# Kernel optimization log

Measured on AMD Instinct MI355X. Metric: run time of the kernel, lower is better.

The kernel has to match this reference:

```python
import jax, jax.numpy as jnp
import numpy as np
import math

B, T, DM = 2, 2048, 2048
H, D = 16, 128
HALF = D // 2


def _rope_tables(T, half, base=10000.0):
    inv_freq = 1.0 / (base ** (np.arange(0, half, dtype=np.float32) / half))
    t = np.arange(T, dtype=np.float32)
    freqs = np.outer(t, inv_freq)  # [T, half]
    return jnp.asarray(np.cos(freqs)), jnp.asarray(np.sin(freqs))


def setup_inputs() -> dict:
    key = jax.random.key(0)
    ks = jax.random.split(key, 5)
    s = 1.0 / math.sqrt(DM)
    x = jax.random.normal(ks[0], (B, T, DM), dtype=jnp.float32)
    wq = jax.random.normal(ks[1], (H * D, DM), dtype=jnp.float32) * s
    wk = jax.random.normal(ks[2], (H * D, DM), dtype=jnp.float32) * s
    wv = jax.random.normal(ks[3], (H * D, DM), dtype=jnp.float32) * s
    wo = jax.random.normal(ks[4], (DM, H * D), dtype=jnp.float32) * s
    cos, sin = _rope_tables(T, HALF)
    return {"x": x, "wq": wq, "wk": wk, "wv": wv, "wo": wo, "cos": cos, "sin": sin}


def _apply_rope(x, cos, sin):
    # x: [B,H,T,D]; cos/sin: [T, D//2] broadcast over batch and head
    x1, x2 = x[..., :HALF], x[..., HALF:]
    c = cos[None, None]
    s = sin[None, None]
    return jnp.concatenate([x1 * c - x2 * s, x1 * s + x2 * c], axis=-1)


def reference(x, wq, wk, wv, wo, cos, sin):
    Bx, Tx, _ = x.shape
    # QKV projections (Linear with weight [out,in]): y = x @ W^T
    q = jnp.einsum('btd,ed->bte', x, wq).reshape(Bx, Tx, H, D).transpose(0, 2, 1, 3)
    k = jnp.einsum('btd,ed->bte', x, wk).reshape(Bx, Tx, H, D).transpose(0, 2, 1, 3)
    v = jnp.einsum('btd,ed->bte', x, wv).reshape(Bx, Tx, H, D).transpose(0, 2, 1, 3)
    q = _apply_rope(q, cos, sin)
    k = _apply_rope(k, cos, sin)
    # causal SDPA (prefill path: kv_cache=None, mask='causal')
    scale = 1.0 / math.sqrt(D)
    scores = jnp.einsum('bhqd,bhkd->bhqk', q, k) * scale  # [B,H,T,T]
    causal = jnp.tril(jnp.ones((Tx, Tx), dtype=bool))
    scores = jnp.where(causal[None, None], scores, jnp.finfo(scores.dtype).min)
    attn = jax.nn.softmax(scores, axis=-1)
    out = jnp.einsum('bhqk,bhkd->bhqd', attn, v)  # [B,H,T,D]
    out = out.transpose(0, 2, 1, 3).reshape(Bx, Tx, H * D)
    return jnp.einsum('bte,de->btd', out, wo)
```

## Files before the change

kernel.cpp:

```cpp
#include <hip/hip_runtime.h>

typedef __attribute__((ext_vector_type(8))) short short8;
typedef __attribute__((ext_vector_type(4))) float floatx4;

#define B_ 2
#define T_ 2048
#define DM_ 2048
#define H_ 16
#define D_ 128
#define HALF_ 64

__device__ inline unsigned short f2bf(float f) {
    union { float f; unsigned u; } v; v.f = f;
    unsigned r = (v.u + 0x7fffu + ((v.u >> 16) & 1u)) >> 16;
    return (unsigned short)r;
}

__device__ inline void gld16(const void* g, void* l) {
    __builtin_amdgcn_global_load_lds(
        (__attribute__((address_space(1))) void*)g,
        (__attribute__((address_space(3))) void*)l,
        16, 0, 0);
}

__global__ void conv_all(const float* __restrict__ x,
                         const float* __restrict__ w0, const float* __restrict__ w1,
                         const float* __restrict__ w2, const float* __restrict__ w3,
                         unsigned short* __restrict__ xb,
                         unsigned short* __restrict__ wb, int n4w) {
    int y = blockIdx.y;
    int i = blockIdx.x * 256 + threadIdx.x;
    const float* src;
    ushort4* dst;
    if (y < 2) { src = x + (size_t)y * n4w * 4; dst = (ushort4*)xb + (size_t)y * n4w; }
    else {
        src = (y == 2) ? w0 : (y == 3) ? w1 : (y == 4) ? w2 : w3;
        dst = (ushort4*)wb + (size_t)(y - 2) * n4w;
    }
    float4 f = ((const float4*)src)[i];
    ushort4 o;
    o.x = f2bf(f.x); o.y = f2bf(f.y); o.z = f2bf(f.z); o.w = f2bf(f.w);
    dst[i] = o;
}

__global__ __launch_bounds__(256)
void gemm_qkv(const unsigned short* __restrict__ A,
              const unsigned short* __restrict__ W,
              unsigned short* __restrict__ q,
              unsigned short* __restrict__ k,
              unsigned short* __restrict__ vt,
              const float* __restrict__ cosT,
              const float* __restrict__ sinT) {
    __shared__ unsigned short sh[18432];
    unsigned short* As = sh;
    unsigned short* Bs = sh + 8192;

    const int t    = threadIdx.x;
    const int lane = t & 63;
    const int w    = t >> 6;
    const int wm   = w >> 1, wn = w & 1;
    const int l15  = lane & 15, quad = lane >> 4;
    const int bx   = blockIdx.x;
    const int row0 = blockIdx.y * 128;
    const int colg0 = bx * 128;
    const int h     = bx & 15;
    const int K = DM_;

    floatx4 acc[4][4];
    for (int i = 0; i < 4; ++i)
        for (int j = 0; j < 4; ++j)
            acc[i][j] = (floatx4){0.f, 0.f, 0.f, 0.f};

    for (int kt = 0; kt < K / 64; ++kt) {
        if (kt) __syncthreads();
        for (int i = 0; i < 4; ++i) {
            int g  = i * 256 + t;
            int g0 = i * 256 + (t & ~63);
            int m  = g >> 3, c = g & 7;
            int k8 = c ^ (m & 7);
            gld16(A + (size_t)(row0 + m) * K + kt * 64 + k8 * 8, As + (size_t)g0 * 8);
            gld16(W + (size_t)(colg0 + m) * K + kt * 64 + k8 * 8, Bs + (size_t)g0 * 8);
        }
        __syncthreads();

        for (int s = 0; s < 2; ++s) {
            short8 a[4], b[4];
            for (int mf = 0; mf < 4; ++mf) {
                int row = wm * 64 + mf * 16 + l15;
                int pc  = (quad + s * 4) ^ (row & 7);
                a[mf] = *(const short8*)(As + row * 64 + pc * 8);
            }
            for (int nf = 0; nf < 4; ++nf) {
                int row = wn * 32 + (nf & 1) * 16 + (nf >> 1) * 64 + l15;
                int pc  = (quad + s * 4) ^ (row & 7);
                b[nf] = *(const short8*)(Bs + row * 64 + pc * 8);
            }
            for (int mf = 0; mf < 4; ++mf)
                for (int nf = 0; nf < 4; ++nf)
                    acc[mf][nf] = __builtin_amdgcn_mfma_f32_16x16x32_bf16(
                        a[mf], b[nf], acc[mf][nf], 0, 0, 0);
        }
    }

    if (bx < 32) {
        unsigned short* C = (bx < 16) ? q : k;
        for (int mf = 0; mf < 4; ++mf) {
            for (int nf = 0; nf < 2; ++nf) {
                int dh = wn * 32 + nf * 16 + l15;
                for (int r = 0; r < 4; ++r) {
                    int rowg = row0 + wm * 64 + mf * 16 + quad * 4 + r;
                    int tt = rowg & 2047;
                    float c = cosT[tt * 64 + dh];
                    float s = sinT[tt * 64 + dh];
                    float x1 = acc[mf][nf][r];
                    float x2 = acc[mf][nf + 2][r];
                    size_t base = (size_t)rowg * DM_ + h * D_ + dh;
                    C[base]         = f2bf(x1 * c - x2 * s);
                    C[base + HALF_] = f2bf(x1 * s + x2 * c);
                }
            }
        }
    } else {
        __syncthreads();
        unsigned short* P = sh + w * 4608;
        for (int mf = 0; mf < 4; ++mf)
            for (int nf = 0; nf < 4; ++nf) {
                int lc = nf * 16 + l15;
                ushort4 o4;
                o4.x = f2bf(acc[mf][nf][0]); o4.y = f2bf(acc[mf][nf][1]);
                o4.z = f2bf(acc[mf][nf][2]); o4.w = f2bf(acc[mf][nf][3]);
                *(ushort4*)(P + lc * 72 + mf * 16 + quad * 4) = o4;
            }
        __syncthreads();
        const int b  = row0 >> 11;
        const int t0 = (row0 & 2047) + wm * 64;
        for (int it = 0; it < 8; ++it) {
            int cidx = it * 64 + lane;
            int lc = cidx >> 3, t8 = cidx & 7;
            int dh = wn * 32 + ((lc >> 4) & 1) * 16 + (lc >> 5) * 64 + (lc & 15);
            uint4 d = *(const uint4*)(P + lc * 72 + t8 * 8);
            *(uint4*)(vt + ((size_t)(b * 16 + h) * 128 + dh) * T_ + t0 + t8 * 8) = d;
        }
    }
}

__global__ __launch_bounds__(256)
void gemm_bt(const unsigned short* __restrict__ A,
             const unsigned short* __restrict__ W,
             float* __restrict__ C, int M, int N, int K) {
    __shared__ unsigned short As[128 * 64];
    __shared__ unsigned short Bs[128 * 64];

    const int t    = threadIdx.x;
    const int lane = t & 63;
    const int w    = t >> 6;
    const int wm   = w >> 1, wn = w & 1;
    const int l15  = lane & 15, quad = lane >> 4;
    const int row0 = blockIdx.y * 128, col0 = blockIdx.x * 128;

    floatx4 acc[4][4];
    for (int i = 0; i < 4; ++i)
        for (int j = 0; j < 4; ++j)
            acc[i][j] = (floatx4){0.f, 0.f, 0.f, 0.f};

    const int nkt = K >> 6;
    for (int kt = 0; kt < nkt; ++kt) {
        if (kt) __syncthreads();
        for (int i = 0; i < 4; ++i) {
            int g  = i * 256 + t;
            int g0 = i * 256 + (t & ~63);
            int m  = g >> 3, c = g & 7;
            int k8 = c ^ (m & 7);
            gld16(A + (size_t)(row0 + m) * K + kt * 64 + k8 * 8,
                  (unsigned short*)As + (size_t)g0 * 8);
            gld16(W + (size_t)(col0 + m) * K + kt * 64 + k8 * 8,
                  (unsigned short*)Bs + (size_t)g0 * 8);
        }
        __syncthreads();

        for (int s = 0; s < 2; ++s) {
            short8 a[4], b[4];
            for (int mf = 0; mf < 4; ++mf) {
                int row = wm * 64 + mf * 16 + l15;
                int pc  = (quad + s * 4) ^ (row & 7);
                a[mf] = *(const short8*)(As + row * 64 + pc * 8);
            }
            for (int nf = 0; nf < 4; ++nf) {
                int row = wn * 64 + nf * 16 + l15;
                int pc  = (quad + s * 4) ^ (row & 7);
                b[nf] = *(const short8*)(Bs + row * 64 + pc * 8);
            }
            for (int mf = 0; mf < 4; ++mf)
                for (int nf = 0; nf < 4; ++nf)
                    acc[mf][nf] = __builtin_amdgcn_mfma_f32_16x16x32_bf16(
                        a[mf], b[nf], acc[mf][nf], 0, 0, 0);
        }
    }

    for (int mf = 0; mf < 4; ++mf)
        for (int nf = 0; nf < 4; ++nf)
            for (int r = 0; r < 4; ++r) {
                int row = row0 + wm * 64 + mf * 16 + quad * 4 + r;
                int col = col0 + wn * 64 + nf * 16 + l15;
                C[(size_t)row * N + col] = acc[mf][nf][r];
            }
}

__global__ __launch_bounds__(256)
void attn_kernel(const unsigned short* __restrict__ q,
                 const unsigned short* __restrict__ k,
                 const unsigned short* __restrict__ vt,
                 unsigned short* __restrict__ ao) {
    __shared__ unsigned short Ks[64 * 128];
    __shared__ unsigned short Vts[128 * 64];
    __shared__ unsigned short Pw[4][16 * 72];

    const int t    = threadIdx.x;
    const int lane = t & 63, w = t >> 6;
    const int l15  = lane & 15, quad = lane >> 4;
    const int j    = blockIdx.x;
    const int bh   = blockIdx.y;
    const int b    = bh >> 4, h = bh & 15;
    const int qt[2] = {31 - j, j};

    const size_t hoff  = (size_t)h * D_;
    const size_t bbase = (size_t)b * T_ * DM_;

    short8 qa[2][4];
    for (int rs = 0; rs < 2; ++rs) {
        const int qw = qt[rs] * 64 + w * 16;
        const unsigned short* qp = q + bbase + (size_t)(qw + l15) * DM_ + hoff + quad * 8;
        for (int ds = 0; ds < 4; ++ds)
            qa[rs][ds] = *(const short8*)(qp + ds * 32);
    }

    floatx4 o[2][8];
    floatx4 lacc[2];
    for (int rs = 0; rs < 2; ++rs) {
        for (int c = 0; c < 8; ++c) o[rs][c] = (floatx4){0.f, 0.f, 0.f, 0.f};
        lacc[rs] = (floatx4){0.f, 0.f, 0.f, 0.f};
    }
    const unsigned short one_bf = 0x3F80;
    short8 ones;
    for (int i = 0; i < 8; ++i) ones[i] = (short)one_bf;

    const float kS = 0.08838834764831845f;
    const int ktend = qt[0];

    for (int kt = 0; kt <= ktend; ++kt) {
        if (kt) __syncthreads();
        for (int i = 0; i < 4; ++i) {
            int it = w * 4 + i;
            int krow = it * 4 + (lane >> 4);
            int gck  = ((lane & 15) ^ (krow & 7));
            gld16(k + bbase + (size_t)(kt * 64 + krow) * DM_ + hoff + gck * 8,
                  (unsigned short*)Ks + it * 512);
            int vrow = it * 8 + (lane >> 3);
            int gcv  = ((lane & 7) ^ (vrow & 7));
            gld16(vt + ((size_t)bh * 128 + vrow) * T_ + kt * 64 + gcv * 8,
                  (unsigned short*)Vts + it * 512);
        }
        __syncthreads();

        for (int rs = 0; rs < 2; ++rs) {
            const int kd = qt[rs];
            if (kt > kd) continue;
            const int qw = qt[rs] * 64 + w * 16;

            floatx4 s[4];
            for (int f = 0; f < 4; ++f) s[f] = (floatx4){0.f, 0.f, 0.f, 0.f};
            for (int ds = 0; ds < 4; ++ds)
                for (int f = 0; f < 4; ++f) {
                    int krow = f * 16 + l15;
                    int phys = (ds * 4 + quad) ^ (krow & 7);
                    short8 bf = *(const short8*)(Ks + krow * 128 + phys * 8);
                    s[f] = __builtin_amdgcn_mfma_f32_16x16x32_bf16(qa[rs][ds], bf, s[f], 0, 0, 0);
                }

            const bool diag = (kt == kd);
            for (int r = 0; r < 4; ++r) {
                int qrow = qw + quad * 4 + r;
                for (int f = 0; f < 4; ++f) {
                    float x = s[f][r] * kS;
                    float e = __expf(x);
                    if (diag && (kt * 64 + f * 16 + l15 > qrow)) e = 0.f;
                    Pw[w][(quad * 4 + r) * 72 + f * 16 + l15] = f2bf(e);
                }
            }

            short8 pa0 = *(const short8*)(&Pw[w][l15 * 72 + quad * 8]);
            short8 pa1 = *(const short8*)(&Pw[w][l15 * 72 + 32 + quad * 8]);
            lacc[rs] = __builtin_amdgcn_mfma_f32_16x16x32_bf16(pa0, ones, lacc[rs], 0, 0, 0);
            lacc[rs] = __builtin_amdgcn_mfma_f32_16x16x32_bf16(pa1, ones, lacc[rs], 0, 0, 0);
            for (int c = 0; c < 8; ++c) {
                int vrow = c * 16 + l15;
                short8 b0 = *(const short8*)(Vts + vrow * 64 + ((quad) ^ (vrow & 7)) * 8);
                short8 b1 = *(const short8*)(Vts + vrow * 64 + ((4 + quad) ^ (vrow & 7)) * 8);
                o[rs][c] = __builtin_amdgcn_mfma_f32_16x16x32_bf16(pa0, b0, o[rs][c], 0, 0, 0);
                o[rs][c] = __builtin_amdgcn_mfma_f32_16x16x32_bf16(pa1, b1, o[rs][c], 0, 0, 0);
            }
        }
    }

    for (int rs = 0; rs < 2; ++rs) {
        const int qw = qt[rs] * 64 + w * 16;
        for (int r = 0; r < 4; ++r) {
            float inv = 1.0f / lacc[rs][r];
            int qrow = qw + quad * 4 + r;
            size_t obase = bbase + (size_t)qrow * DM_ + hoff;
            for (int c = 0; c < 8; ++c)
                ao[obase + c * 16 + l15] = f2bf(o[rs][c][r] * inv);
        }
    }
}

extern "C" void kernel_launch(void* const* d_in, const int* in_sizes, int n_in,
                              void* d_out, int out_size, void* d_ws, size_t ws_size,
                              hipStream_t stream) {
    const float* x    = (const float*)d_in[0];
    const float* wq   = (const float*)d_in[1];
    const float* wk   = (const float*)d_in[2];
    const float* wv   = (const float*)d_in[3];
    const float* wo   = (const float*)d_in[4];
    const float* cosT = (const float*)d_in[5];
    const float* sinT = (const float*)d_in[6];
    float* out = (float*)d_out;

    const size_t NX = (size_t)B_ * T_ * DM_;
    const size_t NW = (size_t)DM_ * DM_;

    unsigned short* xb  = (unsigned short*)d_ws;
    unsigned short* wqb = xb + NX;
    unsigned short* wob = wqb + 3 * NW;
    unsigned short* qb  = wob + NW;
    unsigned short* kb  = qb + NX;
    unsigned short* vtb = kb + NX;
    unsigned short* aob = vtb + NX;

    conv_all<<<dim3((int)(NW / 4 / 256), 6), 256, 0, stream>>>(
        x, wq, wk, wv, wo, xb, wqb, (int)(NW / 4));

    gemm_qkv<<<dim3(48, 32), 256, 0, stream>>>(xb, wqb, qb, kb, vtb, cosT, sinT);

    attn_kernel<<<dim3(16, B_ * H_), 256, 0, stream>>>(qb, kb, vtb, aob);

    gemm_bt<<<dim3(16, 32), 256, 0, stream>>>(aob, wob, out, B_ * T_, DM_, DM_);
}
```

Baseline: 356.1 us.

## Double-buffer K/V tiles in attention kernel to overlap loads with compute

```diff
diff --git a/kernel.cpp b/kernel.cpp
--- a/kernel.cpp
+++ b/kernel.cpp
@@ -211,8 +211,8 @@
                  const unsigned short* __restrict__ k,
                  const unsigned short* __restrict__ vt,
                  unsigned short* __restrict__ ao) {
-    __shared__ unsigned short Ks[64 * 128];
-    __shared__ unsigned short Vts[128 * 64];
+    __shared__ unsigned short Ks[2][64 * 128];
+    __shared__ unsigned short Vts[2][128 * 64];
     __shared__ unsigned short Pw[4][16 * 72];
 
     const int t    = threadIdx.x;
@@ -247,20 +247,32 @@
     const float kS = 0.08838834764831845f;
     const int ktend = qt[0];
 
+#define STAGE_KV(ktn, bb_)                                                     \
+    { _Pragma("unroll") for (int i = 0; i < 4; ++i) {                          \
+        int it = w * 4 + i;                                                    \
+        int krow = it * 4 + (lane >> 4);                                       \
+        int gck  = ((lane & 15) ^ (krow & 7));                                 \
+        gld16(k + bbase + (size_t)((ktn) * 64 + krow) * DM_ + hoff + gck * 8,  \
+              (unsigned short*)Ks[bb_] + it * 512);                            \
+        int vrow = it * 8 + (lane >> 3);                                       \
+        int gcv  = ((lane & 7) ^ (vrow & 7));                                  \
+        gld16(vt + ((size_t)bh * 128 + vrow) * T_ + (ktn) * 64 + gcv * 8,      \
+              (unsigned short*)Vts[bb_] + it * 512); } }
+
+    STAGE_KV(0, 0)
+
     for (int kt = 0; kt <= ktend; ++kt) {
-        if (kt) __syncthreads();
-        for (int i = 0; i < 4; ++i) {
-            int it = w * 4 + i;
-            int krow = it * 4 + (lane >> 4);
-            int gck  = ((lane & 15) ^ (krow & 7));
-            gld16(k + bbase + (size_t)(kt * 64 + krow) * DM_ + hoff + gck * 8,
-                  (unsigned short*)Ks + it * 512);
-            int vrow = it * 8 + (lane >> 3);
-            int gcv  = ((lane & 7) ^ (vrow & 7));
-            gld16(vt + ((size_t)bh * 128 + vrow) * T_ + kt * 64 + gcv * 8,
-                  (unsigned short*)Vts + it * 512);
-        }
-        __syncthreads();
+        const int cb = kt & 1, nb = cb ^ 1;
+
+        __builtin_amdgcn_s_barrier();
+        if (kt < ktend) {
+            STAGE_KV(kt + 1, nb)
+            asm volatile("s_waitcnt vmcnt(8)" ::: "memory");
+        } else {
+            asm volatile("s_waitcnt vmcnt(0)" ::: "memory");
+        }
+        __builtin_amdgcn_s_barrier();
+        __builtin_amdgcn_sched_barrier(0);
 
         for (int rs = 0; rs < 2; ++rs) {
             const int kd = qt[rs];
@@ -273,7 +285,7 @@
                 for (int f = 0; f < 4; ++f) {
                     int krow = f * 16 + l15;
                     int phys = (ds * 4 + quad) ^ (krow & 7);
-                    short8 bf = *(const short8*)(Ks + krow * 128 + phys * 8);
+                    short8 bf = *(const short8*)(Ks[cb] + krow * 128 + phys * 8);
                     s[f] = __builtin_amdgcn_mfma_f32_16x16x32_bf16(qa[rs][ds], bf, s[f], 0, 0, 0);
                 }
 
@@ -294,13 +306,14 @@
             lacc[rs] = __builtin_amdgcn_mfma_f32_16x16x32_bf16(pa1, ones, lacc[rs], 0, 0, 0);
             for (int c = 0; c < 8; ++c) {
                 int vrow = c * 16 + l15;
-                short8 b0 = *(const short8*)(Vts + vrow * 64 + ((quad) ^ (vrow & 7)) * 8);
-                short8 b1 = *(const short8*)(Vts + vrow * 64 + ((4 + quad) ^ (vrow & 7)) * 8);
+                short8 b0 = *(const short8*)(Vts[cb] + vrow * 64 + ((quad) ^ (vrow & 7)) * 8);
+                short8 b1 = *(const short8*)(Vts[cb] + vrow * 64 + ((4 + quad) ^ (vrow & 7)) * 8);
                 o[rs][c] = __builtin_amdgcn_mfma_f32_16x16x32_bf16(pa0, b0, o[rs][c], 0, 0, 0);
                 o[rs][c] = __builtin_amdgcn_mfma_f32_16x16x32_bf16(pa1, b1, o[rs][c], 0, 0, 0);
             }
         }
     }
+#undef STAGE_KV
 
     for (int rs = 0; rs < 2; ++rs) {
         const int qw = qt[rs] * 64 + w * 16;
```

Measured after the change: 356.4 us. Within noise of the previous version (+0.1%).

## Interleave both query tiles in attention loop to share K/V fragment loads

Applied to the files above, without the earlier changes.

```diff
diff --git a/kernel.cpp b/kernel.cpp
--- a/kernel.cpp
+++ b/kernel.cpp
@@ -206,14 +206,14 @@
             }
 }
 
-__global__ __launch_bounds__(256)
+__global__ __launch_bounds__(256, 3)
 void attn_kernel(const unsigned short* __restrict__ q,
                  const unsigned short* __restrict__ k,
                  const unsigned short* __restrict__ vt,
                  unsigned short* __restrict__ ao) {
     __shared__ unsigned short Ks[64 * 128];
     __shared__ unsigned short Vts[128 * 64];
-    __shared__ unsigned short Pw[4][16 * 72];
+    __shared__ unsigned short Pw[2][4][16 * 72];
 
     const int t    = threadIdx.x;
     const int lane = t & 63, w = t >> 6;
@@ -244,7 +244,7 @@
     short8 ones;
     for (int i = 0; i < 8; ++i) ones[i] = (short)one_bf;
 
-    const float kS = 0.08838834764831845f;
+    const float kS2 = 0.12751707470412752f;
     const int ktend = qt[0];
 
     for (int kt = 0; kt <= ktend; ++kt) {
@@ -262,44 +262,102 @@
         }
         __syncthreads();
 
-        for (int rs = 0; rs < 2; ++rs) {
-            const int kd = qt[rs];
-            if (kt > kd) continue;
-            const int qw = qt[rs] * 64 + w * 16;
-
-            floatx4 s[4];
-            for (int f = 0; f < 4; ++f) s[f] = (floatx4){0.f, 0.f, 0.f, 0.f};
+        const bool act1 = (kt <= qt[1]);
+
+        floatx4 s0[4], s1[4];
+        for (int f = 0; f < 4; ++f) {
+            s0[f] = (floatx4){0.f, 0.f, 0.f, 0.f};
+            s1[f] = (floatx4){0.f, 0.f, 0.f, 0.f};
+        }
+        __builtin_amdgcn_s_setprio(1);
+        if (act1) {
+#pragma unroll
             for (int ds = 0; ds < 4; ++ds)
+#pragma unroll
                 for (int f = 0; f < 4; ++f) {
                     int krow = f * 16 + l15;
                     int phys = (ds * 4 + quad) ^ (krow & 7);
                     short8 bf = *(const short8*)(Ks + krow * 128 + phys * 8);
-                    s[f] = __builtin_amdgcn_mfma_f32_16x16x32_bf16(qa[rs][ds], bf, s[f], 0, 0, 0);
+                    s0[f] = __builtin_amdgcn_mfma_f32_16x16x32_bf16(qa[0][ds], bf, s0[f], 0, 0, 0);
+                    s1[f] = __builtin_amdgcn_mfma_f32_16x16x32_bf16(qa[1][ds], bf, s1[f], 0, 0, 0);
                 }
-
-            const bool diag = (kt == kd);
+        } else {
+#pragma unroll
+            for (int ds = 0; ds < 4; ++ds)
+#pragma unroll
+                for (int f = 0; f < 4; ++f) {
+                    int krow = f * 16 + l15;
+                    int phys = (ds * 4 + quad) ^ (krow & 7);
+                    short8 bf = *(const short8*)(Ks + krow * 128 + phys * 8);
+                    s0[f] = __builtin_amdgcn_mfma_f32_16x16x32_bf16(qa[0][ds], bf, s0[f], 0, 0, 0);
+                }
+        }
+        __builtin_amdgcn_s_setprio(0);
+
+        {
+            const bool diag0 = (kt == qt[0]);
+            const int qw0 = qt[0] * 64 + w * 16;
+#pragma unroll
             for (int r = 0; r < 4; ++r) {
-                int qrow = qw + quad * 4 + r;
+                int qrow = qw0 + quad * 4 + r;
+#pragma unroll
                 for (int f = 0; f < 4; ++f) {
-                    float x = s[f][r] * kS;
-                    float e = __expf(x);
-                    if (diag && (kt * 64 + f * 16 + l15 > qrow)) e = 0.f;
-                    Pw[w][(quad * 4 + r) * 72 + f * 16 + l15] = f2bf(e);
+                    float e = exp2f(s0[f][r] * kS2);
+                    if (diag0 && (kt * 64 + f * 16 + l15 > qrow)) e = 0.f;
+                    Pw[0][w][(quad * 4 + r) * 72 + f * 16 + l15] = f2bf(e);
                 }
             }
-
-            short8 pa0 = *(const short8*)(&Pw[w][l15 * 72 + quad * 8]);
-            short8 pa1 = *(const short8*)(&Pw[w][l15 * 72 + 32 + quad * 8]);
-            lacc[rs] = __builtin_amdgcn_mfma_f32_16x16x32_bf16(pa0, ones, lacc[rs], 0, 0, 0);
-            lacc[rs] = __builtin_amdgcn_mfma_f32_16x16x32_bf16(pa1, ones, lacc[rs], 0, 0, 0);
+        }
+        if (act1) {
+            const bool diag1 = (kt == qt[1]);
+            const int qw1 = qt[1] * 64 + w * 16;
+#pragma unroll
+            for (int r = 0; r < 4; ++r) {
+                int qrow = qw1 + quad * 4 + r;
+#pragma unroll
+                for (int f = 0; f < 4; ++f) {
+                    float e = exp2f(s1[f][r] * kS2);
+                    if (diag1 && (kt * 64 + f * 16 + l15 > qrow)) e = 0.f;
+                    Pw[1][w][(quad * 4 + r) * 72 + f * 16 + l15] = f2bf(e);
+                }
+            }
+        }
+
+        short8 pa00 = *(const short8*)(&Pw[0][w][l15 * 72 + quad * 8]);
+        short8 pa01 = *(const short8*)(&Pw[0][w][l15 * 72 + 32 + quad * 8]);
+        lacc[0] = __builtin_amdgcn_mfma_f32_16x16x32_bf16(pa00, ones, lacc[0], 0, 0, 0);
+        lacc[0] = __builtin_amdgcn_mfma_f32_16x16x32_bf16(pa01, ones, lacc[0], 0, 0, 0);
+        short8 pa10, pa11;
+        if (act1) {
+            pa10 = *(const short8*)(&Pw[1][w][l15 * 72 + quad * 8]);
+            pa11 = *(const short8*)(&Pw[1][w][l15 * 72 + 32 + quad * 8]);
+            lacc[1] = __builtin_amdgcn_mfma_f32_16x16x32_bf16(pa10, ones, lacc[1], 0, 0, 0);
+            lacc[1] = __builtin_amdgcn_mfma_f32_16x16x32_bf16(pa11, ones, lacc[1], 0, 0, 0);
+        }
+
+        __builtin_amdgcn_s_setprio(1);
+        if (act1) {
+#pragma unroll
             for (int c = 0; c < 8; ++c) {
                 int vrow = c * 16 + l15;
                 short8 b0 = *(const short8*)(Vts + vrow * 64 + ((quad) ^ (vrow & 7)) * 8);
                 short8 b1 = *(const short8*)(Vts + vrow * 64 + ((4 + quad) ^ (vrow & 7)) * 8);
-                o[rs][c] = __builtin_amdgcn_mfma_f32_16x16x32_bf16(pa0, b0, o[rs][c], 0, 0, 0);
-                o[rs][c] = __builtin_amdgcn_mfma_f32_16x16x32_bf16(pa1, b1, o[rs][c], 0, 0, 0);
-            }
-        }
+                o[0][c] = __builtin_amdgcn_mfma_f32_16x16x32_bf16(pa00, b0, o[0][c], 0, 0, 0);
+                o[0][c] = __builtin_amdgcn_mfma_f32_16x16x32_bf16(pa01, b1, o[0][c], 0, 0, 0);
+                o[1][c] = __builtin_amdgcn_mfma_f32_16x16x32_bf16(pa10, b0, o[1][c], 0, 0, 0);
+                o[1][c] = __builtin_amdgcn_mfma_f32_16x16x32_bf16(pa11, b1, o[1][c], 0, 0, 0);
+            }
+        } else {
+#pragma unroll
+            for (int c = 0; c < 8; ++c) {
+                int vrow = c * 16 + l15;
+                short8 b0 = *(const short8*)(Vts + vrow * 64 + ((quad) ^ (vrow & 7)) * 8);
+                short8 b1 = *(const short8*)(Vts + vrow * 64 + ((4 + quad) ^ (vrow & 7)) * 8);
+                o[0][c] = __builtin_amdgcn_mfma_f32_16x16x32_bf16(pa00, b0, o[0][c], 0, 0, 0);
+                o[0][c] = __builtin_amdgcn_mfma_f32_16x16x32_bf16(pa01, b1, o[0][c], 0, 0, 0);
+            }
+        }
+        __builtin_amdgcn_s_setprio(0);
     }
 
     for (int rs = 0; rs < 2; ++rs) {
```

Result: slower. 541.1 us (+51.9%).

## Assign one query tile per block instead of pairing tiles, add MFMA priority hints

Applied to the files above, without the earlier changes.

```diff
diff --git a/kernel.cpp b/kernel.cpp
--- a/kernel.cpp
+++ b/kernel.cpp
@@ -218,36 +218,32 @@
     const int t    = threadIdx.x;
     const int lane = t & 63, w = t >> 6;
     const int l15  = lane & 15, quad = lane >> 4;
-    const int j    = blockIdx.x;
+    const int qt   = 31 - blockIdx.x;
     const int bh   = blockIdx.y;
     const int b    = bh >> 4, h = bh & 15;
-    const int qt[2] = {31 - j, j};
 
     const size_t hoff  = (size_t)h * D_;
     const size_t bbase = (size_t)b * T_ * DM_;
-
-    short8 qa[2][4];
-    for (int rs = 0; rs < 2; ++rs) {
-        const int qw = qt[rs] * 64 + w * 16;
+    const int qw = qt * 64 + w * 16;
+
+    short8 qa[4];
+    {
         const unsigned short* qp = q + bbase + (size_t)(qw + l15) * DM_ + hoff + quad * 8;
         for (int ds = 0; ds < 4; ++ds)
-            qa[rs][ds] = *(const short8*)(qp + ds * 32);
-    }
-
-    floatx4 o[2][8];
-    floatx4 lacc[2];
-    for (int rs = 0; rs < 2; ++rs) {
-        for (int c = 0; c < 8; ++c) o[rs][c] = (floatx4){0.f, 0.f, 0.f, 0.f};
-        lacc[rs] = (floatx4){0.f, 0.f, 0.f, 0.f};
-    }
+            qa[ds] = *(const short8*)(qp + ds * 32);
+    }
+
+    floatx4 o[8];
+    floatx4 lacc = (floatx4){0.f, 0.f, 0.f, 0.f};
+    for (int c = 0; c < 8; ++c) o[c] = (floatx4){0.f, 0.f, 0.f, 0.f};
+
     const unsigned short one_bf = 0x3F80;
     short8 ones;
     for (int i = 0; i < 8; ++i) ones[i] = (short)one_bf;
 
-    const float kS = 0.08838834764831845f;
-    const int ktend = qt[0];
-
-    for (int kt = 0; kt <= ktend; ++kt) {
+    const float kS2 = 0.12751707470412752f;
+
+    for (int kt = 0; kt <= qt; ++kt) {
         if (kt) __syncthreads();
         for (int i = 0; i < 4; ++i) {
             int it = w * 4 + i;
@@ -262,55 +258,55 @@
         }
         __syncthreads();
 
-        for (int rs = 0; rs < 2; ++rs) {
-            const int kd = qt[rs];
-            if (kt > kd) continue;
-            const int qw = qt[rs] * 64 + w * 16;
-
-            floatx4 s[4];
-            for (int f = 0; f < 4; ++f) s[f] = (floatx4){0.f, 0.f, 0.f, 0.f};
-            for (int ds = 0; ds < 4; ++ds)
-                for (int f = 0; f < 4; ++f) {
-                    int krow = f * 16 + l15;
-                    int phys = (ds * 4 + quad) ^ (krow & 7);
-                    short8 bf = *(const short8*)(Ks + krow * 128 + phys * 8);
-                    s[f] = __builtin_amdgcn_mfma_f32_16x16x32_bf16(qa[rs][ds], bf, s[f], 0, 0, 0);
-                }
-
-            const bool diag = (kt == kd);
-            for (int r = 0; r < 4; ++r) {
-                int qrow = qw + quad * 4 + r;
-                for (int f = 0; f < 4; ++f) {
-                    float x = s[f][r] * kS;
-                    float e = __expf(x);
-                    if (diag && (kt * 64 + f * 16 + l15 > qrow)) e = 0.f;
-                    Pw[w][(quad * 4 + r) * 72 + f * 16 + l15] = f2bf(e);
-                }
-            }
-
-            short8 pa0 = *(const short8*)(&Pw[w][l15 * 72 + quad * 8]);
-            short8 pa1 = *(const short8*)(&Pw[w][l15 * 72 + 32 + quad * 8]);
-            lacc[rs] = __builtin_amdgcn_mfma_f32_16x16x32_bf16(pa0, ones, lacc[rs], 0, 0, 0);
-            lacc[rs] = __builtin_amdgcn_mfma_f32_16x16x32_bf16(pa1, ones, lacc[rs], 0, 0, 0);
-            for (int c = 0; c < 8; ++c) {
-                int vrow = c * 16 + l15;
-                short8 b0 = *(const short8*)(Vts + vrow * 64 + ((quad) ^ (vrow & 7)) * 8);
-                short8 b1 = *(const short8*)(Vts + vrow * 64 + ((4 + quad) ^ (vrow & 7)) * 8);
-                o[rs][c] = __builtin_amdgcn_mfma_f32_16x16x32_bf16(pa0, b0, o[rs][c], 0, 0, 0);
-                o[rs][c] = __builtin_amdgcn_mfma_f32_16x16x32_bf16(pa1, b1, o[rs][c], 0, 0, 0);
-            }
-        }
-    }
-
-    for (int rs = 0; rs < 2; ++rs) {
-        const int qw = qt[rs] * 64 + w * 16;
+        floatx4 s[4];
+        for (int f = 0; f < 4; ++f) s[f] = (floatx4){0.f, 0.f, 0.f, 0.f};
+        __builtin_amdgcn_s_setprio(1);
+#pragma unroll
+        for (int ds = 0; ds < 4; ++ds)
+#pragma unroll
+            for (int f = 0; f < 4; ++f) {
+                int krow = f * 16 + l15;
+                int phys = (ds * 4 + quad) ^ (krow & 7);
+                short8 bf = *(const short8*)(Ks + krow * 128 + phys * 8);
+                s[f] = __builtin_amdgcn_mfma_f32_16x16x32_bf16(qa[ds], bf, s[f], 0, 0, 0);
+            }
+        __builtin_amdgcn_s_setprio(0);
+
+        const bool diag = (kt == qt);
+#pragma unroll
         for (int r = 0; r < 4; ++r) {
-            float inv = 1.0f / lacc[rs][r];
             int qrow = qw + quad * 4 + r;
-            size_t obase = bbase + (size_t)qrow * DM_ + hoff;
-            for (int c = 0; c < 8; ++c)
-                ao[obase + c * 16 + l15] = f2bf(o[rs][c][r] * inv);
-        }
+#pragma unroll
+            for (int f = 0; f < 4; ++f) {
+                float e = exp2f(s[f][r] * kS2);
+                if (diag && (kt * 64 + f * 16 + l15 > qrow)) e = 0.f;
+                Pw[w][(quad * 4 + r) * 72 + f * 16 + l15] = f2bf(e);
+            }
+        }
+
+        short8 pa0 = *(const short8*)(&Pw[w][l15 * 72 + quad * 8]);
+        short8 pa1 = *(const short8*)(&Pw[w][l15 * 72 + 32 + quad * 8]);
+        lacc = __builtin_amdgcn_mfma_f32_16x16x32_bf16(pa0, ones, lacc, 0, 0, 0);
+        lacc = __builtin_amdgcn_mfma_f32_16x16x32_bf16(pa1, ones, lacc, 0, 0, 0);
+
+        __builtin_amdgcn_s_setprio(1);
+#pragma unroll
+        for (int c = 0; c < 8; ++c) {
+            int vrow = c * 16 + l15;
+            short8 b0 = *(const short8*)(Vts + vrow * 64 + ((quad) ^ (vrow & 7)) * 8);
+            short8 b1 = *(const short8*)(Vts + vrow * 64 + ((4 + quad) ^ (vrow & 7)) * 8);
+            o[c] = __builtin_amdgcn_mfma_f32_16x16x32_bf16(pa0, b0, o[c], 0, 0, 0);
+            o[c] = __builtin_amdgcn_mfma_f32_16x16x32_bf16(pa1, b1, o[c], 0, 0, 0);
+        }
+        __builtin_amdgcn_s_setprio(0);
+    }
+
+    for (int r = 0; r < 4; ++r) {
+        float inv = 1.0f / lacc[r];
+        int qrow = qw + quad * 4 + r;
+        size_t obase = bbase + (size_t)qrow * DM_ + hoff;
+        for (int c = 0; c < 8; ++c)
+            ao[obase + c * 16 + l15] = f2bf(o[c][r] * inv);
     }
 }
 
@@ -342,7 +338,7 @@
 
     gemm_qkv<<<dim3(48, 32), 256, 0, stream>>>(xb, wqb, qb, kb, vtb, cosT, sinT);
 
-    attn_kernel<<<dim3(16, B_ * H_), 256, 0, stream>>>(qb, kb, vtb, aob);
+    attn_kernel<<<dim3(32, B_ * H_), 256, 0, stream>>>(qb, kb, vtb, aob);
 
     gemm_bt<<<dim3(16, 32), 256, 0, stream>>>(aob, wob, out, B_ * T_, DM_, DM_);
 }
```

Measured after the change: 416.0 us. 1.17x slower.
